# Kernel tuning notes

Hardware: AMD Instinct MI355X
Metric: run time of the kernel (lower is better)

## Reference

```python
import jax, jax.numpy as jnp
import numpy as np

SIGMA = 0.1

def setup_inputs() -> dict:
    key = jax.random.key(0)
    k1, k2, k3 = jax.random.split(key, 3)
    B, N, M, D = 1, 12288, 12288, 16
    x = jax.random.normal(k1, (B, N, 3), dtype=jnp.float32)
    y = jax.random.normal(k2, (B, M, 3), dtype=jnp.float32)
    y_fea = jax.random.normal(k3, (B, M, D), dtype=jnp.float32)
    return {"x": x, "y": y, "y_fea": y_fea}

def reference(x, y, y_fea):
    # Normalized Gaussian kernel conv (KeOps 'normalized_gauss'):
    # out[b,i] = softmax_j( -||x_i - y_j||^2 / (2*sigma^2) ) @ y_fea[b]
    inv2s2 = 1.0 / (2.0 * SIGMA * SIGMA)
    x2 = jnp.sum(x * x, axis=-1)                      # [B,N]
    y2 = jnp.sum(y * y, axis=-1)                      # [B,M]
    xy = jnp.einsum('bnd,bmd->bnm', x, y)             # [B,N,M]
    d2 = x2[:, :, None] + y2[:, None, :] - 2.0 * xy   # squared distances
    logits = -d2 * inv2s2                             # [B,N,M]
    w = jax.nn.softmax(logits, axis=-1)               # normalized Gaussian weights
    return jnp.einsum('bnm,bmd->bnd', w, y_fea)       # [B,N,D]
```

## Files before the change

### kernel.cpp

```cpp
#include <hip/hip_runtime.h>
#include <hip/hip_bf16.h>


#define NROWS 12288
#define MCOLS 12288
#define DFEA  16
#define CC 72.13475204444817f

typedef __attribute__((ext_vector_type(8))) short bf16x8;
typedef __attribute__((ext_vector_type(4))) float f32x4;
typedef __attribute__((ext_vector_type(2))) float f32x2;

#if __has_builtin(__builtin_amdgcn_exp2f)
#define EXP2(x) __builtin_amdgcn_exp2f(x)
#else
#define EXP2(x) exp2f(x)
#endif

__device__ __forceinline__ f32x2 sp2(float v) { return (f32x2){v, v}; }
__device__ __forceinline__ f32x2 fma2(f32x2 a, f32x2 b, f32x2 c) {
    return __builtin_elementwise_fma(a, b, c);
}
__device__ __forceinline__ f32x2 max2(f32x2 a, f32x2 b) {
    return __builtin_elementwise_max(a, b);
}

__device__ __forceinline__ unsigned enc_f(float f) {
    unsigned u = __float_as_uint(f);
    return u ^ ((unsigned)((int)u >> 31) | 0x80000000u);
}
__device__ __forceinline__ float dec_f(unsigned u) {
    unsigned b = (u & 0x80000000u) ? (u ^ 0x80000000u) : ~u;
    return __uint_as_float(b);
}

__device__ __forceinline__ unsigned pk_bf16(float a, float b) {
    unsigned ua = __float_as_uint(a) + 0x8000u;
    unsigned ub = __float_as_uint(b) + 0x8000u;
    return __builtin_amdgcn_perm(ub, ua, 0x07060302);
}

__global__ __launch_bounds__(256) void fused1_kernel(const float* __restrict__ x,
                                                     const float* __restrict__ y,
                                                     const float* __restrict__ fea,
                                                     uint4* __restrict__ feaB,
                                                     unsigned* __restrict__ Gpart) {
    __shared__ float sh[3584];
    int b = blockIdx.x, t = threadIdx.x;
    if (b < 96) {
        float* fs = sh;
        int j0 = b * 128;
        const float4* src = (const float4*)(fea + (size_t)j0 * DFEA);
        float4* dst = (float4*)fs;
        dst[t] = src[t];
        dst[t + 256] = src[t + 256];
        __syncthreads();
        int tile = t >> 6, lane = t & 63;
        int jb = tile * 32 + ((lane >> 4) << 3);
        int col = lane & 15;
        float v[8];
        #pragma unroll
        for (int jj = 0; jj < 8; ++jj) v[jj] = fs[(jb + jj) * DFEA + col];
        uint4 o;
        o.x = pk_bf16(v[0], v[1]); o.y = pk_bf16(v[2], v[3]);
        o.z = pk_bf16(v[4], v[5]); o.w = pk_bf16(v[6], v[7]);
        feaB[b * 256 + t] = o;
    } else {
        float* s0 = sh; float* s1 = sh + 768; float* s2 = sh + 1536; float* sw = sh + 2304;
        unsigned* redmax = (unsigned*)(sh + 3072);
        int bb = b - 96;
        int rb = bb >> 4;
        int jc = bb & 15;
        int j0 = jc * 768;

        for (int i = t; i < 768; i += 256) {
            float a = y[3 * (j0 + i) + 0];
            float c = y[3 * (j0 + i) + 1];
            float d = y[3 * (j0 + i) + 2];
            s0[i] = 2.0f * CC * a; s1[i] = 2.0f * CC * c; s2[i] = 2.0f * CC * d;
            sw[i] = -CC * (a * a + c * c + d * d);
        }
        redmax[t] = 0u; redmax[t + 256] = 0u;
        __syncthreads();

        int wv   = t >> 6;
        int lane = t & 63;
        int jw   = wv * 192;

        float X0[8], X1[8], X2[8];
        f32x2 mk[8];
        #pragma unroll
        for (int k = 0; k < 8; ++k) {
            int row = rb * 512 + lane + 64 * k;
            X0[k] = x[3 * row + 0]; X1[k] = x[3 * row + 1]; X2[k] = x[3 * row + 2];
            mk[k] = sp2(-3.4e38f);
        }

        for (int jj = jw; jj < jw + 192; jj += 4) {
            f32x4 a0 = *(const f32x4*)&s0[jj];
            f32x4 a1 = *(const f32x4*)&s1[jj];
            f32x4 a2 = *(const f32x4*)&s2[jj];
            f32x4 aw = *(const f32x4*)&sw[jj];
            #pragma unroll
            for (int k = 0; k < 8; ++k) {
                f32x2 g = fma2(sp2(X2[k]), a2.xy, aw.xy);
                g = fma2(sp2(X1[k]), a1.xy, g);
                g = fma2(sp2(X0[k]), a0.xy, g);
                mk[k] = max2(mk[k], g);
                f32x2 h = fma2(sp2(X2[k]), a2.zw, aw.zw);
                h = fma2(sp2(X1[k]), a1.zw, h);
                h = fma2(sp2(X0[k]), a0.zw, h);
                mk[k] = max2(mk[k], h);
            }
        }
        #pragma unroll
        for (int k = 0; k < 8; ++k)
            atomicMax(&redmax[lane + 64 * k], enc_f(fmaxf(mk[k].x, mk[k].y)));
        __syncthreads();
        Gpart[jc * NROWS + rb * 512 + t]       = redmax[t];
        Gpart[jc * NROWS + rb * 512 + t + 256] = redmax[t + 256];
    }
}

template <int CH>
__global__ __launch_bounds__(256, 4) void kacc_kernel(const float* __restrict__ x,
                                                      const float* __restrict__ y,
                                                      const uint4* __restrict__ feaB,
                                                      const unsigned* __restrict__ Gpart,
                                                      float* __restrict__ spart,
                                                      float* __restrict__ apart) {
    constexpr int JPB = MCOLS / CH;
    constexpr int KT  = JPB / 32;
    __shared__ float Ys0[JPB], Ys1[JPB], Ys2[JPB], Ysw[JPB];
    int t  = threadIdx.x;
    int rb = blockIdx.x / CH;
    int jc = blockIdx.x % CH;
    int j0 = jc * JPB;

    for (int i = t; i < JPB; i += 256) {
        float a = y[3 * (j0 + i) + 0];
        float c = y[3 * (j0 + i) + 1];
        float d = y[3 * (j0 + i) + 2];
        Ys0[i] = 2.0f * CC * a; Ys1[i] = 2.0f * CC * c; Ys2[i] = 2.0f * CC * d;
        Ysw[i] = -CC * (a * a + c * c + d * d);
    }
    __syncthreads();

    int wv   = t >> 6;
    int lane = t & 63;
    int grp  = lane >> 4;
    int m    = lane & 15;
    int rowbase = rb * 256 + wv * 64;

    float X0[4], X1[4], X2[4], Gm[4];
    #pragma unroll
    for (int r = 0; r < 4; ++r) {
        int row = rowbase + r * 16 + m;
        X0[r] = x[3 * row + 0]; X1[r] = x[3 * row + 1]; X2[r] = x[3 * row + 2];
        unsigned ge = 0u;
        #pragma unroll
        for (int c = 0; c < 16; ++c) ge = max(ge, Gpart[c * NROWS + row]);
        Gm[r] = dec_f(ge);
    }

    const uint4* fb = feaB + (size_t)jc * (JPB * 2) + lane;

    const bf16x8 ones = (bf16x8){(short)0x3F80, (short)0x3F80, (short)0x3F80, (short)0x3F80,
                                 (short)0x3F80, (short)0x3F80, (short)0x3F80, (short)0x3F80};
    f32x4 acc[4], accs[4];
    #pragma unroll
    for (int r = 0; r < 4; ++r) {
        acc[r]  = (f32x4){0.f, 0.f, 0.f, 0.f};
        accs[r] = (f32x4){0.f, 0.f, 0.f, 0.f};
    }

    for (int kt = 0; kt < KT; ++kt) {
        int jb = kt * 32 + grp * 8;
        f32x4 A0 = *(const f32x4*)&Ys0[jb], B0 = *(const f32x4*)&Ys0[jb + 4];
        f32x4 A1 = *(const f32x4*)&Ys1[jb], B1 = *(const f32x4*)&Ys1[jb + 4];
        f32x4 A2 = *(const f32x4*)&Ys2[jb], B2 = *(const f32x4*)&Ys2[jb + 4];
        f32x4 Aw = *(const f32x4*)&Ysw[jb], Bw = *(const f32x4*)&Ysw[jb + 4];
        bf16x8 bfrag = __builtin_bit_cast(bf16x8, fb[kt * 64]);

        #pragma unroll
        for (int r = 0; r < 4; ++r) {
            f32x2 x0 = sp2(X0[r]), x1 = sp2(X1[r]), x2 = sp2(X2[r]);
            f32x2 gm = sp2(Gm[r]);
            f32x2 g0 = fma2(x0, A0.xy, fma2(x1, A1.xy, fma2(x2, A2.xy, Aw.xy))) - gm;
            f32x2 g1 = fma2(x0, A0.zw, fma2(x1, A1.zw, fma2(x2, A2.zw, Aw.zw))) - gm;
            f32x2 g2 = fma2(x0, B0.xy, fma2(x1, B1.xy, fma2(x2, B2.xy, Bw.xy))) - gm;
            f32x2 g3 = fma2(x0, B0.zw, fma2(x1, B1.zw, fma2(x2, B2.zw, Bw.zw))) - gm;
            union { unsigned u[4]; bf16x8 v; } af;
            af.u[0] = pk_bf16(EXP2(g0.x), EXP2(g0.y));
            af.u[1] = pk_bf16(EXP2(g1.x), EXP2(g1.y));
            af.u[2] = pk_bf16(EXP2(g2.x), EXP2(g2.y));
            af.u[3] = pk_bf16(EXP2(g3.x), EXP2(g3.y));
            acc[r]  = __builtin_amdgcn_mfma_f32_16x16x32_bf16(af.v, bfrag, acc[r], 0, 0, 0);
            accs[r] = __builtin_amdgcn_mfma_f32_16x16x32_bf16(af.v, ones,  accs[r], 0, 0, 0);
        }
    }

    float* ap = apart + (size_t)jc * (NROWS * DFEA);
    #pragma unroll
    for (int r = 0; r < 4; ++r) {
        #pragma unroll
        for (int reg = 0; reg < 4; ++reg) {
            int orow = rowbase + r * 16 + grp * 4 + reg;
            ap[(size_t)orow * DFEA + m] = acc[r][reg];
        }
        if (m == 0) {
            #pragma unroll
            for (int reg = 0; reg < 4; ++reg)
                spart[jc * NROWS + rowbase + r * 16 + grp * 4 + reg] = accs[r][reg];
        }
    }
}

template <int CH>
__global__ __launch_bounds__(256) void kdiv_kernel(const float* __restrict__ spart,
                                                   const float* __restrict__ apart,
                                                   float* __restrict__ out) {
    int tid = blockIdx.x * 256 + threadIdx.x;
    int row = tid >> 4;
    float s = 0.0f;
    #pragma unroll
    for (int c = 0; c < CH; ++c) s += spart[c * NROWS + row];
    float o = 0.0f;
    #pragma unroll
    for (int c = 0; c < CH; ++c) o += apart[(size_t)c * (NROWS * DFEA) + tid];
    out[tid] = o / s;
}

extern "C" void kernel_launch(void* const* d_in, const int* in_sizes, int n_in,
                              void* d_out, int out_size, void* d_ws, size_t ws_size,
                              hipStream_t stream) {
    const float* x   = (const float*)d_in[0];
    const float* y   = (const float*)d_in[1];
    const float* fea = (const float*)d_in[2];
    float* out = (float*)d_out;

    float*    wsf   = (float*)d_ws;
    unsigned* Gpart = (unsigned*)wsf;

    const size_t need16 = ((size_t)16 * NROWS + (size_t)16 * NROWS + 98304 +
                           (size_t)16 * NROWS * DFEA) * 4;

    if (ws_size >= need16) {
        constexpr int CH = 16;
        float* spart = wsf + 16 * NROWS;
        uint4* feaB  = (uint4*)(wsf + 16 * NROWS + CH * NROWS);
        float* apart = wsf + 16 * NROWS + CH * NROWS + 98304;
        fused1_kernel<<<dim3(480), 256, 0, stream>>>(x, y, fea, feaB, Gpart);
        kacc_kernel<CH><<<dim3(48 * CH), 256, 0, stream>>>(x, y, feaB, Gpart, spart, apart);
        kdiv_kernel<CH><<<dim3(768), 256, 0, stream>>>(spart, apart, out);
    } else {
        constexpr int CH = 4;
        float* spart = wsf + 16 * NROWS;
        uint4* feaB  = (uint4*)(wsf + 16 * NROWS + CH * NROWS);
        float* apart = wsf + 16 * NROWS + CH * NROWS + 98304;
        fused1_kernel<<<dim3(480), 256, 0, stream>>>(x, y, fea, feaB, Gpart);
        kacc_kernel<CH><<<dim3(48 * CH), 256, 0, stream>>>(x, y, feaB, Gpart, spart, apart);
        kdiv_kernel<CH><<<dim3(768), 256, 0, stream>>>(spart, apart, out);
    }
}
```

Measured before the change: 111.9 us.

## Precompute scaled y terms globally, drop LDS staging, raise split count to 32

The first kernel now also writes the scaled y coordinates and weight terms to global workspace in separate arrays. The accumulation kernel reads them directly from global or L2 instead of staging them in shared memory with a barrier, and its inner loop is unrolled by two. When workspace allows, the column split grows from 16 to 32 chunks to launch more blocks. In exchange, the inner loop now pays global load latency, and the final division kernel has more partial sums to reduce.

```diff
diff --git a/kernel.cpp b/kernel.cpp
--- a/kernel.cpp
+++ b/kernel.cpp
@@ -44,6 +44,10 @@
                                                      const float* __restrict__ y,
                                                      const float* __restrict__ fea,
                                                      uint4* __restrict__ feaB,
+                                                     float* __restrict__ ys0,
+                                                     float* __restrict__ ys1,
+                                                     float* __restrict__ ys2,
+                                                     float* __restrict__ ysw,
                                                      unsigned* __restrict__ Gpart) {
     __shared__ float sh[3584];
     int b = blockIdx.x, t = threadIdx.x;
@@ -65,10 +69,17 @@
         o.x = pk_bf16(v[0], v[1]); o.y = pk_bf16(v[2], v[3]);
         o.z = pk_bf16(v[4], v[5]); o.w = pk_bf16(v[6], v[7]);
         feaB[b * 256 + t] = o;
+    } else if (b < 144) {
+        int j = (b - 96) * 256 + t;
+        float a = y[3 * j + 0], c = y[3 * j + 1], d = y[3 * j + 2];
+        ys0[j] = 2.0f * CC * a;
+        ys1[j] = 2.0f * CC * c;
+        ys2[j] = 2.0f * CC * d;
+        ysw[j] = -CC * (a * a + c * c + d * d);
     } else {
         float* s0 = sh; float* s1 = sh + 768; float* s2 = sh + 1536; float* sw = sh + 2304;
         unsigned* redmax = (unsigned*)(sh + 3072);
-        int bb = b - 96;
+        int bb = b - 144;
         int rb = bb >> 4;
         int jc = bb & 15;
         int j0 = jc * 768;
@@ -124,27 +135,20 @@
 
 template <int CH>
 __global__ __launch_bounds__(256, 4) void kacc_kernel(const float* __restrict__ x,
-                                                      const float* __restrict__ y,
+                                                      const float* __restrict__ ys0,
+                                                      const float* __restrict__ ys1,
+                                                      const float* __restrict__ ys2,
+                                                      const float* __restrict__ ysw,
                                                       const uint4* __restrict__ feaB,
                                                       const unsigned* __restrict__ Gpart,
                                                       float* __restrict__ spart,
                                                       float* __restrict__ apart) {
     constexpr int JPB = MCOLS / CH;
     constexpr int KT  = JPB / 32;
-    __shared__ float Ys0[JPB], Ys1[JPB], Ys2[JPB], Ysw[JPB];
     int t  = threadIdx.x;
     int rb = blockIdx.x / CH;
     int jc = blockIdx.x % CH;
     int j0 = jc * JPB;
-
-    for (int i = t; i < JPB; i += 256) {
-        float a = y[3 * (j0 + i) + 0];
-        float c = y[3 * (j0 + i) + 1];
-        float d = y[3 * (j0 + i) + 2];
-        Ys0[i] = 2.0f * CC * a; Ys1[i] = 2.0f * CC * c; Ys2[i] = 2.0f * CC * d;
-        Ysw[i] = -CC * (a * a + c * c + d * d);
-    }
-    __syncthreads();
 
     int wv   = t >> 6;
     int lane = t & 63;
@@ -174,12 +178,13 @@
         accs[r] = (f32x4){0.f, 0.f, 0.f, 0.f};
     }
 
+    #pragma unroll 2
     for (int kt = 0; kt < KT; ++kt) {
-        int jb = kt * 32 + grp * 8;
-        f32x4 A0 = *(const f32x4*)&Ys0[jb], B0 = *(const f32x4*)&Ys0[jb + 4];
-        f32x4 A1 = *(const f32x4*)&Ys1[jb], B1 = *(const f32x4*)&Ys1[jb + 4];
-        f32x4 A2 = *(const f32x4*)&Ys2[jb], B2 = *(const f32x4*)&Ys2[jb + 4];
-        f32x4 Aw = *(const f32x4*)&Ysw[jb], Bw = *(const f32x4*)&Ysw[jb + 4];
+        int jb = j0 + kt * 32 + grp * 8;
+        f32x4 A0 = *(const f32x4*)&ys0[jb], B0 = *(const f32x4*)&ys0[jb + 4];
+        f32x4 A1 = *(const f32x4*)&ys1[jb], B1 = *(const f32x4*)&ys1[jb + 4];
+        f32x4 A2 = *(const f32x4*)&ys2[jb], B2 = *(const f32x4*)&ys2[jb + 4];
+        f32x4 Aw = *(const f32x4*)&ysw[jb], Bw = *(const f32x4*)&ysw[jb + 4];
         bf16x8 bfrag = __builtin_bit_cast(bf16x8, fb[kt * 64]);
 
         #pragma unroll
@@ -241,25 +246,25 @@
 
     float*    wsf   = (float*)d_ws;
     unsigned* Gpart = (unsigned*)wsf;
-
-    const size_t need16 = ((size_t)16 * NROWS + (size_t)16 * NROWS + 98304 +
-                           (size_t)16 * NROWS * DFEA) * 4;
-
-    if (ws_size >= need16) {
-        constexpr int CH = 16;
-        float* spart = wsf + 16 * NROWS;
-        uint4* feaB  = (uint4*)(wsf + 16 * NROWS + CH * NROWS);
-        float* apart = wsf + 16 * NROWS + CH * NROWS + 98304;
-        fused1_kernel<<<dim3(480), 256, 0, stream>>>(x, y, fea, feaB, Gpart);
-        kacc_kernel<CH><<<dim3(48 * CH), 256, 0, stream>>>(x, y, feaB, Gpart, spart, apart);
+    float*    ys0   = wsf + 16 * NROWS;
+    float*    ys1   = ys0 + NROWS;
+    float*    ys2   = ys1 + NROWS;
+    float*    ysw   = ys2 + NROWS;
+
+    auto run = [&](auto chc) {
+        constexpr int CH = decltype(chc)::value;
+        float* spart = wsf + 20 * NROWS;
+        uint4* feaB  = (uint4*)(spart + CH * NROWS);
+        float* apart = (float*)feaB + 98304;
+        fused1_kernel<<<dim3(528), 256, 0, stream>>>(x, y, fea, feaB,
+                                                     ys0, ys1, ys2, ysw, Gpart);
+        kacc_kernel<CH><<<dim3(48 * CH), 256, 0, stream>>>(x, ys0, ys1, ys2, ysw,
+                                                           feaB, Gpart, spart, apart);
         kdiv_kernel<CH><<<dim3(768), 256, 0, stream>>>(spart, apart, out);
-    } else {
-        constexpr int CH = 4;
-        float* spart = wsf + 16 * NROWS;
-        uint4* feaB  = (uint4*)(wsf + 16 * NROWS + CH * NROWS);
-        float* apart = wsf + 16 * NROWS + CH * NROWS + 98304;
-        fused1_kernel<<<dim3(480), 256, 0, stream>>>(x, y, fea, feaB, Gpart);
-        kacc_kernel<CH><<<dim3(48 * CH), 256, 0, stream>>>(x, y, feaB, Gpart, spart, apart);
-        kdiv_kernel<CH><<<dim3(768), 256, 0, stream>>>(spart, apart, out);
-    }
-}
+    };
+
+    const size_t need32 = ((size_t)20 * NROWS + 32 * NROWS + 98304 +
+                           (size_t)32 * NROWS * DFEA) * 4;
+    if (ws_size >= need32) run(std::integral_constant<int, 32>{});
+    else                   run(std::integral_constant<int, 16>{});
+}
```

Result: slower. 126.3 us (+12.9%).
